# Kernel tuning notes

Hardware: AMD Instinct MI355X
Metric: run time of the kernel (lower is better)

## Reference

```python
import jax, jax.numpy as jnp
import numpy as np

T = 20            # time_steps
BETA = 0.85
THR = 1.0         # snntorch Leaky default threshold
A_PRE = 0.005
A_POST = -0.003
STDP_INT = 3


@jax.custom_vjp
def spike_fn(mem_shift):
    # heaviside spike; backward uses snntorch atan surrogate (alpha=2)
    return (mem_shift > 0).astype(mem_shift.dtype)

def _spk_fwd(m):
    return (m > 0).astype(m.dtype), m

def _spk_bwd(m, g):
    # snntorch surrogate.atan, alpha=2: grad = g * (alpha/2) / (1 + (pi/2*alpha*U)^2) = g / (1 + (pi*U)^2)
    return (g / (1.0 + (jnp.pi * m) ** 2),)

spike_fn.defvjp(_spk_fwd, _spk_bwd)


def _lif(cur, mem):
    # snntorch Leaky (reset-by-subtraction): reset from previous mem (detached)
    reset = jax.lax.stop_gradient((mem > THR).astype(cur.dtype))
    mem = BETA * mem + cur - reset * THR
    spk = spike_fn(mem - THR)
    return spk, mem


def _snn_forward(x, embed, W1, b1, W2, b2, W3, b3, Wout, bout):
    B, S = x.shape
    H = W1.shape[0]
    x_emb = jnp.transpose(embed[x], (1, 0, 2))   # [S,B,E]
    x_rep = jnp.repeat(x_emb, T, axis=0)         # [S*T,B,E] (same embed for all 20 steps of a token)

    def step(carry, xe):
        mem1, mem2, mem3 = carry
        spk1, mem1 = _lif(xe @ W1.T + b1, mem1)
        spk2, mem2 = _lif(spk1 @ W2.T + b2, mem2)
        spk3, mem3 = _lif(spk2 @ W3.T + b3, mem3)
        return (mem1, mem2, mem3), (spk1, spk2, spk3)

    z = jnp.zeros((B, H), x_emb.dtype)
    (mem1, mem2, mem3), (spk1a, spk2a, spk3a) = jax.lax.scan(step, (z, z, z), x_rep)

    # STDP accumulation on steps where step % 3 == 0 (no-grad in original)
    mask = jnp.tile((jnp.arange(T) % STDP_INT == 0).astype(x_emb.dtype), S)  # [S*T]

    def stdp(pre, post):
        pre_m = jax.lax.stop_gradient(pre.mean(axis=1))    # [N, in]
        post_m = jax.lax.stop_gradient(post.mean(axis=1))  # [N, out]
        return jnp.einsum('n,no,ni->oi', mask, A_POST * post_m, A_PRE * pre_m)

    d1 = stdp(x_rep, spk1a)
    d2 = stdp(spk1a, spk2a)
    d3 = stdp(spk2a, spk3a)

    pooled = spk3a.reshape(S, T, B, H).mean(axis=1)  # mean over time_steps -> [S,B,H]
    out = jnp.transpose(pooled @ Wout.T + bout, (1, 0, 2))  # [B,S,V]
    rec1, rec2, rec3 = (jax.lax.stop_gradient(s) for s in (spk1a, spk2a, spk3a))
    return out, mem1, mem2, mem3, d1, d2, d3, rec1, rec2, rec3


def setup_inputs() -> dict:
    key = jax.random.key(0)
    ks = jax.random.split(key, 10)
    V, H, E, B, S = 32000, 256, 128, 32, 128
    inp = {
        'x': jax.random.randint(ks[0], (B, S), 0, V),
        'embed': jax.random.normal(ks[1], (V, E), jnp.float32),
        'W1': jax.random.normal(ks[2], (H, E), jnp.float32) * 0.08,
        'b1': jnp.zeros((H,), jnp.float32),
        'W2': jax.random.normal(ks[3], (H, H), jnp.float32) * 0.06,
        'b2': jnp.zeros((H,), jnp.float32),
        'W3': jax.random.normal(ks[4], (H, H), jnp.float32) * 0.06,
        'b3': jnp.zeros((H,), jnp.float32),
        'Wout': jax.random.normal(ks[5], (V, H), jnp.float32) * 0.06,
        'bout': jnp.zeros((V,), jnp.float32),
    }
    return inp


def reference(x, embed, W1, b1, W2, b2, W3, b3, Wout, bout):
    return _snn_forward(x, embed, W1, b1, W2, b2, W3, b3, Wout, bout)
```

## Files before the change

### kernel.cpp

```cpp
#include <hip/hip_runtime.h>
#include <cstdint>

#define T_STEPS 20
#define S_LEN   128
#define BATCH   32
#define HID     256
#define EMB     128
#define VOCAB   32000
#define NSTEP   (S_LEN*T_STEPS)
#define NBROWS  (NSTEP*BATCH)

typedef __bf16 bf8   __attribute__((ext_vector_type(8)));
typedef float  f32x4 __attribute__((ext_vector_type(4)));

static __device__ __forceinline__ unsigned short f2bf_u(float f){
  unsigned int u = __builtin_bit_cast(unsigned int, f);
  u = u + 0x7FFFu + ((u >> 16) & 1u);
  return (unsigned short)(u >> 16);
}

__global__ void k_f32_to_bf16(const float* __restrict__ src, unsigned short* __restrict__ dst, int n4){
  int i = blockIdx.x*blockDim.x + threadIdx.x;
  if (i < n4){
    float4 v = ((const float4*)src)[i];
    ushort4 o; o.x=f2bf_u(v.x); o.y=f2bf_u(v.y); o.z=f2bf_u(v.z); o.w=f2bf_u(v.w);
    ((ushort4*)dst)[i] = o;
  }
}

__global__ void k_wT(const float* __restrict__ W, float* __restrict__ WT){
  int i = blockIdx.x*blockDim.x + threadIdx.x;
  int n = i >> 8, k = i & 255;
  WT[k*HID + n] = W[i];
}

__global__ void k_xm(const int* __restrict__ x, const float* __restrict__ embed, float* __restrict__ Xm){
  int s = blockIdx.x, i = threadIdx.x;
  float acc = 0.f;
  for (int b=0;b<BATCH;b++){
    int tok = x[b*S_LEN + s];
    acc += embed[(size_t)tok*EMB + i];
  }
  Xm[s*EMB + i] = acc * (1.0f/32.0f);
}

__global__ __launch_bounds__(256) void k_cur1(const int* __restrict__ x, const float* __restrict__ embed,
                                              const float* __restrict__ W1, const float* __restrict__ b1,
                                              float* __restrict__ cur1){
  __shared__ float xe[BATCH*EMB];
  int s = blockIdx.x, t = threadIdx.x;
  for (int i=t; i<BATCH*EMB/4; i+=256){
    int b = i >> 5, e4 = i & 31;
    int tok = x[b*S_LEN + s];
    ((float4*)xe)[i] = ((const float4*)(embed + (size_t)tok*EMB))[e4];
  }
  __syncthreads();
  int h = t;
  float acc[BATCH];
  #pragma unroll
  for (int b=0;b<BATCH;b++) acc[b]=0.f;
  for (int ec=0; ec<4; ec++){
    float wd[32];
    #pragma unroll
    for (int e=0;e<32;e++) wd[e] = W1[(size_t)h*EMB + ec*32 + e];
    #pragma unroll
    for (int b=0;b<BATCH;b++){
      #pragma unroll
      for (int e=0;e<32;e++)
        acc[b] = fmaf(xe[b*EMB + ec*32 + e], wd[e], acc[b]);
    }
  }
  float bi = b1[h];
  #pragma unroll
  for (int b=0;b<BATCH;b++)
    cur1[(size_t)(s*BATCH + b)*HID + h] = __fadd_rn(acc[b], bi);
}

__global__ __launch_bounds__(64) void k_scan1(const float* __restrict__ cur1, float* __restrict__ rec,
                                              float* __restrict__ memout){
  int bid = blockIdx.x; int b = bid >> 2; int hq = bid & 3;
  int h = hq*64 + threadIdx.x;
  const int strN = BATCH*HID;
  const float* cp = cur1 + b*HID + h;
  float* rp = rec + b*HID + h;
  float mem = 0.f;
  for (int s=0; s<S_LEN; s++){
    float c = cp[(size_t)s*strN];
    #pragma unroll
    for (int t=0;t<T_STEPS;t++){
      float reset = (mem > 1.0f) ? 1.0f : 0.0f;
      float tm = __fmul_rn(0.85f, mem);
      tm = __fadd_rn(tm, c);
      mem = __fsub_rn(tm, reset);
      rp[(size_t)(s*T_STEPS + t)*strN] = (mem > 1.0f) ? 1.0f : 0.0f;
    }
  }
  memout[b*HID + h] = mem;
}

template<bool POOL>
__global__ __launch_bounds__(64) void k_scan23(const float* __restrict__ cur,
                                               float* __restrict__ rec, float* __restrict__ memout,
                                               unsigned short* __restrict__ pooled){
  int bid = blockIdx.x; int b = bid >> 2; int hq = bid & 3;
  int h = hq*64 + threadIdx.x;
  const int strN = BATCH*HID;
  const float* cp = cur + b*HID + h;
  float* rp = rec + b*HID + h;
  unsigned short* pp = POOL ? (pooled + (size_t)b*S_LEN*HID + h) : nullptr;
  float mem = 0.f;
  float ps = 0.f;
  int tc = 0, sTok = 0;
  float cA[16], cB[16];

  auto step = [&](float c, int n){
    float reset = (mem > 1.0f) ? 1.0f : 0.0f;
    float tm = __fmul_rn(0.85f, mem);
    tm = __fadd_rn(tm, c);
    mem = __fsub_rn(tm, reset);
    float spk = (mem > 1.0f) ? 1.f : 0.f;
    rp[(size_t)n*strN] = spk;
    if constexpr (POOL){
      ps += spk;
      if (++tc == T_STEPS){
        pp[(size_t)sTok*HID] = f2bf_u(__fdiv_rn(ps, 20.0f));
        ps = 0.f; tc = 0; ++sTok;
      }
    }
  };

  #pragma unroll
  for (int j=0;j<16;j++) cA[j] = cp[(size_t)j*strN];
  for (int n0=0; n0<NSTEP; n0+=32){
    #pragma unroll
    for (int j=0;j<16;j++) cB[j] = cp[(size_t)(n0+16+j)*strN];
    #pragma unroll
    for (int j=0;j<16;j++) step(cA[j], n0+j);
    if (n0+32 < NSTEP){
      #pragma unroll
      for (int j=0;j<16;j++) cA[j] = cp[(size_t)(n0+32+j)*strN];
    }
    #pragma unroll
    for (int j=0;j<16;j++) step(cB[j], n0+16+j);
  }
  memout[b*HID + h] = mem;
}

__global__ __launch_bounds__(256) void k_gemm_f32(const float* __restrict__ spk,
                                                  const float* __restrict__ WT,
                                                  const float* __restrict__ bias,
                                                  float* __restrict__ curo){
  int m = blockIdx.x * 256 + threadIdx.x;
  int n0 = blockIdx.y * 16;
  const float* sp = spk + (size_t)m*HID;
  float acc[16];
  #pragma unroll
  for (int i=0;i<16;i++) acc[i]=0.f;
  for (int kc=0; kc<8; kc++){
    float sd[32];
    #pragma unroll
    for (int i=0;i<8;i++){
      float4 v = *(const float4*)(sp + kc*32 + i*4);
      sd[i*4+0]=v.x; sd[i*4+1]=v.y; sd[i*4+2]=v.z; sd[i*4+3]=v.w;
    }
    #pragma unroll
    for (int k=0;k<32;k++){
      float sv = sd[k];
      const float* wt = WT + (size_t)(kc*32+k)*HID + n0;
      #pragma unroll
      for (int n=0;n<16;n++)
        acc[n] = fmaf(sv, wt[n], acc[n]);
    }
  }
  float* op = curo + (size_t)m*HID + n0;
  #pragma unroll
  for (int n=0;n<16;n++) op[n] = __fadd_rn(acc[n], bias[n0+n]);
}

template<bool BF16B>
__global__ __launch_bounds__(256,2) void k_gemm_out(const unsigned short* __restrict__ Abf,
                                                    const unsigned short* __restrict__ Bbf,
                                                    const float* __restrict__ Bf32,
                                                    const float* __restrict__ bout,
                                                    float* __restrict__ outp){
  __shared__ unsigned short As[128*72];
  __shared__ unsigned short Bs[128*72];
  int bid = blockIdx.x;
  int ntile = bid >> 5;
  int mtile = bid & 31;
  int m0 = mtile*128, n0 = ntile*128;
  int tid = threadIdx.x;
  int lane = tid & 63, wave = tid >> 6;
  int wm = wave >> 1, wn = wave & 1;
  int lm = lane & 15, quad = lane >> 4;
  f32x4 acc[4][4] = {};

  for (int kt=0; kt<4; kt++){
    int k0 = kt*64;
    uint4 avb[4];
    #pragma unroll
    for (int i=0;i<4;i++){
      int id = tid + i*256; int r = id>>3, c16 = id&7;
      avb[i] = *(const uint4*)(Abf + (size_t)(m0 + r)*HID + k0 + c16*8);
    }
    uint4 bvb[4]; float4 bvf[8];
    if (BF16B){
      #pragma unroll
      for (int i=0;i<4;i++){
        int id = tid + i*256; int r = id>>3, c16 = id&7;
        bvb[i] = *(const uint4*)(Bbf + (size_t)(n0 + r)*HID + k0 + c16*8);
      }
    } else {
      #pragma unroll
      for (int i=0;i<8;i++){
        int id = tid + i*256; int r = id>>4, c4 = id&15;
        bvf[i] = *(const float4*)(Bf32 + (size_t)(n0 + r)*HID + k0 + c4*4);
      }
    }
    __syncthreads();
    #pragma unroll
    for (int i=0;i<4;i++){
      int id = tid + i*256; int r = id>>3, c16 = id&7;
      *(uint4*)(As + r*72 + c16*8) = avb[i];
    }
    if (BF16B){
      #pragma unroll
      for (int i=0;i<4;i++){
        int id = tid + i*256; int r = id>>3, c16 = id&7;
        *(uint4*)(Bs + r*72 + c16*8) = bvb[i];
      }
    } else {
      #pragma unroll
      for (int i=0;i<8;i++){
        int id = tid + i*256; int r = id>>4, c4 = id&15;
        ushort4 o; o.x=f2bf_u(bvf[i].x); o.y=f2bf_u(bvf[i].y); o.z=f2bf_u(bvf[i].z); o.w=f2bf_u(bvf[i].w);
        *(ushort4*)(Bs + r*72 + c4*4) = o;
      }
    }
    __syncthreads();
    bf8 af[4][2], bfr[4][2];
    #pragma unroll
    for (int mt=0;mt<4;mt++)
      #pragma unroll
      for (int kk=0;kk<2;kk++)
        af[mt][kk] = *(const bf8*)(As + (wm*64 + mt*16 + lm)*72 + kk*32 + quad*8);
    #pragma unroll
    for (int nt=0;nt<4;nt++)
      #pragma unroll
      for (int kk=0;kk<2;kk++)
        bfr[nt][kk] = *(const bf8*)(Bs + (wn*64 + nt*16 + lm)*72 + kk*32 + quad*8);
    #pragma unroll
    for (int mt=0;mt<4;mt++)
      #pragma unroll
      for (int nt=0;nt<4;nt++){
        acc[mt][nt] = __builtin_amdgcn_mfma_f32_16x16x32_bf16(af[mt][0], bfr[nt][0], acc[mt][nt], 0,0,0);
        acc[mt][nt] = __builtin_amdgcn_mfma_f32_16x16x32_bf16(af[mt][1], bfr[nt][1], acc[mt][nt], 0,0,0);
      }
    __syncthreads();
  }
  #pragma unroll
  for (int nt=0;nt<4;nt++){
    int v = n0 + wn*64 + nt*16 + lm;
    float bo = bout[v];
    #pragma unroll
    for (int mt=0;mt<4;mt++)
      #pragma unroll
      for (int rr=0;rr<4;rr++){
        int r = m0 + wm*64 + mt*16 + quad*4 + rr;
        outp[(size_t)r*VOCAB + v] = acc[mt][nt][rr] + bo;
      }
  }
}

__global__ void k_mmean(const float* __restrict__ rec, float* __restrict__ M){
  int m = blockIdx.x, o = threadIdx.x;
  int s = m / 7, j = m - 7*s;
  int n = s*T_STEPS + j*3;
  const float* rp = rec + (size_t)n*BATCH*HID + o;
  float acc = 0.f;
  #pragma unroll
  for (int b=0;b<BATCH;b++) acc += rp[b*HID];
  M[m*HID + o] = acc * (1.0f/32.0f);
}

__global__ void k_d1(const float* __restrict__ M1, const float* __restrict__ Xm, float* __restrict__ d1){
  __shared__ float col[896];
  int o = blockIdx.x, i = threadIdx.x;
  for (int m=i; m<896; m+=128) col[m] = M1[m*HID + o];
  __syncthreads();
  float acc = 0.f;
  for (int s=0;s<S_LEN;s++){
    float xv = Xm[s*EMB + i];
    float cs = 0.f;
    #pragma unroll
    for (int j=0;j<7;j++) cs += col[s*7+j];
    acc += cs * xv;
  }
  d1[o*EMB + i] = -1.5e-5f * acc;
}

__global__ void k_d23(const float* __restrict__ Mpost, const float* __restrict__ Mpre, float* __restrict__ d){
  __shared__ float col[896];
  int o = blockIdx.x, i = threadIdx.x;
  for (int m=i; m<896; m+=256) col[m] = Mpost[m*HID + o];
  __syncthreads();
  float acc = 0.f;
  for (int m=0;m<896;m++) acc += col[m] * Mpre[m*HID + i];
  d[o*HID + i] = -1.5e-5f * acc;
}

extern "C" void kernel_launch(void* const* d_in, const int* in_sizes, int n_in,
                              void* d_out, int out_size, void* d_ws, size_t ws_size,
                              hipStream_t stream){
  const int*   x     = (const int*)d_in[0];
  const float* embed = (const float*)d_in[1];
  const float* W1    = (const float*)d_in[2];
  const float* b1    = (const float*)d_in[3];
  const float* W2    = (const float*)d_in[4];
  const float* b2    = (const float*)d_in[5];
  const float* W3    = (const float*)d_in[6];
  const float* b3    = (const float*)d_in[7];
  const float* Wout  = (const float*)d_in[8];
  const float* bout  = (const float*)d_in[9];
  float* out = (float*)d_out;

  float* mem1 = out + 131072000;
  float* mem2 = out + 131080192;
  float* mem3 = out + 131088384;
  float* d1   = out + 131096576;
  float* d2   = out + 131129344;
  float* d3   = out + 131194880;
  float* rec1 = out + 131260416;
  float* rec2 = out + 152231936;
  float* rec3 = out + 173203456;

  float* curbuf = out + 0;
  float* cur1   = out + 20971520;
  float* Xm     = out + 22020096;
  float* M1     = out + 22036480;
  float* M2     = out + 22265856;
  float* M3     = out + 22495232;
  float* WT2    = out + 22724608;
  float* WT3    = out + 22790144;

  unsigned short* pooled = (unsigned short*)d_ws;
  bool haveWoutBf = ws_size >= (size_t)(2097152 + 16384000);
  unsigned short* woutbf = (unsigned short*)((char*)d_ws + 2097152);

  if (haveWoutBf)
    k_f32_to_bf16<<<8000,256,0,stream>>>(Wout, woutbf, VOCAB*HID/4);
  k_wT<<<256,256,0,stream>>>(W2, WT2);
  k_wT<<<256,256,0,stream>>>(W3, WT3);
  k_xm<<<128,128,0,stream>>>(x, embed, Xm);
  k_cur1<<<128,256,0,stream>>>(x, embed, W1, b1, cur1);

  k_scan1<<<128,64,0,stream>>>(cur1, rec1, mem1);
  k_gemm_f32<<<dim3(320,16),256,0,stream>>>(rec1, WT2, b2, curbuf);
  k_scan23<false><<<128,64,0,stream>>>(curbuf, rec2, mem2, nullptr);
  k_gemm_f32<<<dim3(320,16),256,0,stream>>>(rec2, WT3, b3, curbuf);
  k_scan23<true><<<128,64,0,stream>>>(curbuf, rec3, mem3, pooled);

  k_mmean<<<896,256,0,stream>>>(rec1, M1);
  k_mmean<<<896,256,0,stream>>>(rec2, M2);
  k_mmean<<<896,256,0,stream>>>(rec3, M3);
  k_d1<<<256,128,0,stream>>>(M1, Xm, d1);
  k_d23<<<256,256,0,stream>>>(M2, M1, d2);
  k_d23<<<256,256,0,stream>>>(M3, M2, d3);

  if (haveWoutBf)
    k_gemm_out<true ><<<8000,256,0,stream>>>(pooled, woutbf, nullptr, bout, out);
  else
    k_gemm_out<false><<<8000,256,0,stream>>>(pooled, nullptr, Wout,  bout, out);
}
```

Baseline: 1.948 ms.

## Stage spike rows in LDS for hidden GEMM and widen N tile

The fp32 hidden-layer GEMM now loads each 256-row block's spike rows cooperatively into shared memory with coalesced float4 loads, instead of each thread striding through its own row. Each thread now computes 32 output columns instead of 16, and the grid is swapped so the N tiles of one M block sit next to each other. Smaller tweaks vectorize the W1 loads in k_cur1 and prefetch the next token's current in k_scan1. The cost is extra barriers and LDS traffic plus 32 accumulators per thread, which may reduce occupancy. The weight reads stay broadcast scalar loads.

Result: no change. 1.966 ms (+0.9%).

```diff
diff --git a/kernel.cpp b/kernel.cpp
--- a/kernel.cpp
+++ b/kernel.cpp
@@ -62,7 +62,10 @@
   for (int ec=0; ec<4; ec++){
     float wd[32];
     #pragma unroll
-    for (int e=0;e<32;e++) wd[e] = W1[(size_t)h*EMB + ec*32 + e];
+    for (int e4=0;e4<8;e4++){
+      float4 w = *(const float4*)(W1 + (size_t)h*EMB + ec*32 + e4*4);
+      wd[e4*4+0]=w.x; wd[e4*4+1]=w.y; wd[e4*4+2]=w.z; wd[e4*4+3]=w.w;
+    }
     #pragma unroll
     for (int b=0;b<BATCH;b++){
       #pragma unroll
@@ -84,8 +87,9 @@
   const float* cp = cur1 + b*HID + h;
   float* rp = rec + b*HID + h;
   float mem = 0.f;
+  float c = cp[0];
   for (int s=0; s<S_LEN; s++){
-    float c = cp[(size_t)s*strN];
+    float cn = (s+1 < S_LEN) ? cp[(size_t)(s+1)*strN] : 0.f;
     #pragma unroll
     for (int t=0;t<T_STEPS;t++){
       float reset = (mem > 1.0f) ? 1.0f : 0.0f;
@@ -94,6 +98,7 @@
       mem = __fsub_rn(tm, reset);
       rp[(size_t)(s*T_STEPS + t)*strN] = (mem > 1.0f) ? 1.0f : 0.0f;
     }
+    c = cn;
   }
   memout[b*HID + h] = mem;
 }
@@ -150,31 +155,41 @@
                                                   const float* __restrict__ WT,
                                                   const float* __restrict__ bias,
                                                   float* __restrict__ curo){
-  int m = blockIdx.x * 256 + threadIdx.x;
-  int n0 = blockIdx.y * 16;
-  const float* sp = spk + (size_t)m*HID;
-  float acc[16];
-  #pragma unroll
-  for (int i=0;i<16;i++) acc[i]=0.f;
+  __shared__ float As[256*36];
+  int m0 = blockIdx.y * 256;
+  int n0 = blockIdx.x * 32;
+  int t  = threadIdx.x;
+  float acc[32];
+  #pragma unroll
+  for (int n=0;n<32;n++) acc[n]=0.f;
+
   for (int kc=0; kc<8; kc++){
-    float sd[32];
+    __syncthreads();
     #pragma unroll
     for (int i=0;i<8;i++){
-      float4 v = *(const float4*)(sp + kc*32 + i*4);
-      sd[i*4+0]=v.x; sd[i*4+1]=v.y; sd[i*4+2]=v.z; sd[i*4+3]=v.w;
-    }
-    #pragma unroll
-    for (int k=0;k<32;k++){
-      float sv = sd[k];
-      const float* wt = WT + (size_t)(kc*32+k)*HID + n0;
-      #pragma unroll
-      for (int n=0;n<16;n++)
-        acc[n] = fmaf(sv, wt[n], acc[n]);
-    }
-  }
-  float* op = curo + (size_t)m*HID + n0;
-  #pragma unroll
-  for (int n=0;n<16;n++) op[n] = __fadd_rn(acc[n], bias[n0+n]);
+      int id = t + i*256;
+      int r = id >> 3, c4 = id & 7;
+      float4 v = *(const float4*)(spk + (size_t)(m0 + r)*HID + kc*32 + c4*4);
+      *(float4*)(As + r*36 + c4*4) = v;
+    }
+    __syncthreads();
+    const float* wrow = WT + (size_t)(kc*32)*HID + n0;
+    #pragma unroll
+    for (int g=0; g<8; g++){
+      float4 sv4 = *(const float4*)(As + t*36 + g*4);
+      #pragma unroll
+      for (int j=0;j<4;j++){
+        float sv = (j==0)?sv4.x:(j==1)?sv4.y:(j==2)?sv4.z:sv4.w;
+        const float* wt = wrow + (size_t)(g*4+j)*HID;
+        #pragma unroll
+        for (int n=0;n<32;n++)
+          acc[n] = fmaf(sv, wt[n], acc[n]);
+      }
+    }
+  }
+  float* op = curo + (size_t)(m0 + t)*HID + n0;
+  #pragma unroll
+  for (int n=0;n<32;n++) op[n] = __fadd_rn(acc[n], bias[n0+n]);
 }
 
 template<bool BF16B>
@@ -355,9 +370,9 @@
   k_cur1<<<128,256,0,stream>>>(x, embed, W1, b1, cur1);
 
   k_scan1<<<128,64,0,stream>>>(cur1, rec1, mem1);
-  k_gemm_f32<<<dim3(320,16),256,0,stream>>>(rec1, WT2, b2, curbuf);
+  k_gemm_f32<<<dim3(8,320),256,0,stream>>>(rec1, WT2, b2, curbuf);
   k_scan23<false><<<128,64,0,stream>>>(curbuf, rec2, mem2, nullptr);
-  k_gemm_f32<<<dim3(320,16),256,0,stream>>>(rec2, WT3, b3, curbuf);
+  k_gemm_f32<<<dim3(8,320),256,0,stream>>>(rec2, WT3, b3, curbuf);
   k_scan23<true><<<128,64,0,stream>>>(curbuf, rec3, mem3, pooled);
 
   k_mmean<<<896,256,0,stream>>>(rec1, M1);
```
